# Kernel tuning notes

Hardware: AMD Instinct MI355X
Metric: run time of the kernel (lower is better)

The kernel has to match this reference:

```python
import jax, jax.numpy as jnp
import numpy as np

L = 4          # n_layers
HID = 64       # hidden_channels
MODES = 16     # n_modes
HEADS = 4      # n_heads
NP_SP = 500    # spatial engram patterns
NP_FR = 200    # spectral engram patterns
ED = 8         # embed_dim
WS = 4         # spatial window size
PRIME = 31.0


def setup_inputs() -> dict:
    key = jax.random.key(0)
    ks = jax.random.split(key, 20)
    B, Cin, Cout, S = 16, 3, 1, 16384
    f = lambda k, sh: jax.random.normal(k, sh, dtype=jnp.float32) * 0.05
    ch = HID // HEADS
    return {
        "x": jax.random.normal(ks[0], (B, Cin, S), dtype=jnp.float32),
        "lift_W": f(ks[1], (Cin, HID)), "lift_b": f(ks[2], (HID,)),
        "proj_W": f(ks[3], (HID, Cout)), "proj_b": f(ks[4], (Cout,)),
        "sp_emb": f(ks[5], (L, NP_SP, ED)), "sp_W": f(ks[6], (L, ED, HID)), "sp_b": f(ks[7], (L, HID)),
        "fr_emb": f(ks[8], (L, NP_FR, ED)), "fr_W": f(ks[9], (L, ED, HID * MODES)), "fr_b": f(ks[10], (L, HID * MODES)),
        "g_W1": f(ks[11], (L, 3 * HID, 64)), "g_b1": f(ks[12], (L, 64)),
        "g_W2": f(ks[13], (L, 64, 3)), "g_b2": f(ks[14], (L, 3)),
        "mhf_Wr": f(ks[15], (L, HEADS, ch, ch, MODES)),
        "mhf_Wi": f(ks[16], (L, HEADS, ch, ch, MODES)),
    }


def _spatial_engram(x, emb, W, b):
    # x: [B, C, S] -> hash each replicate-padded window of size WS -> embedding gather -> linear
    B, C, S = x.shape
    pad = WS // 2
    xp = jnp.pad(x, ((0, 0), (0, 0), (pad, pad)), mode='edge')   # [B, C, S+WS]
    sC = xp.sum(axis=1)                                          # [B, S+WS]
    # window sum over WS consecutive positions (vectorized over all seq positions)
    wsum = sC[:, 0:S] + sC[:, 1:S + 1] + sC[:, 2:S + 2] + sC[:, 3:S + 3]  # [B, S]
    idx = (wsum * PRIME).astype(jnp.int32) % NP_SP               # truncate-toward-zero like torch .long()
    idx = jnp.clip(idx, 0, NP_SP - 1)
    e = emb[idx]                                                 # [B, S, ED] gather
    out = e @ W + b                                              # [B, S, C]
    return out.transpose(0, 2, 1)                                # [B, C, S]


def _spectral_engram(x, emb, W, b):
    B, C, S = x.shape
    xf = jnp.fft.rfft(x, axis=-1)                                # [B, C, F]
    mag = jnp.abs(xf[:, :, :MODES]).mean(axis=1)                 # [B, MODES]
    idx = ((mag * 1000.0).astype(jnp.int32)).sum(axis=1) % NP_FR # [B]
    e = emb[idx]                                                 # [B, ED]
    proj = (e @ W + b).reshape(B, C, MODES)
    full = jnp.zeros((B, C, xf.shape[-1]), dtype=xf.dtype).at[:, :, :MODES].set(proj.astype(xf.dtype))
    return jnp.fft.irfft(full, n=S, axis=-1)


def _mhf_spectral_conv(x, Wr, Wi):
    # multi-head Fourier spectral conv: per-head complex channel mixing on low modes
    B, C, S = x.shape
    ch = C // HEADS
    xf = jnp.fft.rfft(x, axis=-1)                                # [B, C, F]
    xh = xf[:, :, :MODES].reshape(B, HEADS, ch, MODES)           # [B, H, ch, M]
    Wc = Wr + 1j * Wi                                            # [H, ch, ch, M]
    of = jnp.einsum('bhim,hiom->bhom', xh, Wc).reshape(B, C, MODES)
    full = jnp.zeros((B, C, xf.shape[-1]), dtype=xf.dtype).at[:, :, :MODES].set(of)
    return jnp.fft.irfft(full, n=S, axis=-1)


def _gated_fusion(sp, mh, fr, W1, b1, W2, b2):
    g = jnp.concatenate([sp.mean(-1), mh.mean(-1), fr.mean(-1)], axis=-1)  # [B, 3C]
    h = jax.nn.relu(g @ W1 + b1)
    w = jax.nn.softmax(h @ W2 + b2, axis=-1)                     # [B, 3]
    return (w[:, 0, None, None] * sp + w[:, 1, None, None] * mh + w[:, 2, None, None] * fr)


def reference(x, lift_W, lift_b, proj_W, proj_b, sp_emb, sp_W, sp_b,
              fr_emb, fr_W, fr_b, g_W1, g_b1, g_W2, g_b2, mhf_Wr, mhf_Wi):
    # lifting: [B, Cin, S] -> [B, HID, S]
    h = jnp.einsum('bcs,cd->bds', x, lift_W) + lift_b[None, :, None]
    for i in range(L):
        sp = _spatial_engram(h, sp_emb[i], sp_W[i], sp_b[i])
        mh = _mhf_spectral_conv(h, mhf_Wr[i], mhf_Wi[i])
        fr = _spectral_engram(h, fr_emb[i], fr_W[i], fr_b[i])
        h = _gated_fusion(sp, mh, fr, g_W1[i], g_b1[i], g_W2[i], g_b2[i])
        h = jax.nn.gelu(h, approximate=False)  # torch F.gelu default = exact erf
    out = jnp.einsum('bcs,cd->bds', h, proj_W) + proj_b[None, :, None]
    return out
```

## Files before the change

### kernel.cpp

```cpp
#include <hip/hip_runtime.h>
#include <math.h>

#define B_ 16
#define CIN_ 3
#define HID_ 64
#define S_ 16384
#define MODES_ 16
#define HEADS_ 4
#define CH_ 16
#define ED_ 8
#define NPSP_ 500
#define NPFR_ 200
#define LAYERS_ 4
#define RECW_ 34

__device__ __forceinline__ float gelu_f32(float v) {
    return 0.5f * v * (1.0f + erff(v * 0.70710678118654752f));
}

__device__ __constant__ double KC_[16] = {1.0, 0.99518472667219688624,
    0.98078528040323044913, 0.95694033573220886494, 0.92387953251128675613,
    0.88192126434835502971, 0.83146961230254523708, 0.77301045336273696081,
    0.70710678118654752440, 0.63439328416364549822, 0.55557023301960222474,
    0.47139673682599764856, 0.38268343236508977173, 0.29028467725446236764,
    0.19509032201612826785, 0.09801714032956060199};
__device__ __constant__ double KS_[16] = {0.0, 0.09801714032956060199,
    0.19509032201612826785, 0.29028467725446236764, 0.38268343236508977173,
    0.47139673682599764856, 0.55557023301960222474, 0.63439328416364549822,
    0.70710678118654752440, 0.77301045336273696081, 0.83146961230254523708,
    0.88192126434835502971, 0.92387953251128675613, 0.95694033573220886494,
    0.98078528040323044913, 0.99518472667219688624};

__global__ __launch_bounds__(256) void k_sptab(const float* __restrict__ sp_emb,
                                               const float* __restrict__ sp_W,
                                               float* __restrict__ T0f) {
    int lay = blockIdx.y;
    int tid = blockIdx.x * 256 + threadIdx.x;
    int c = tid & 63, id = tid >> 6;
    const float* e = sp_emb + (size_t)lay * NPSP_ * ED_ + (size_t)id * ED_;
    const float* w = sp_W + (size_t)lay * ED_ * HID_ + c;
    double a = 0.0;
#pragma unroll
    for (int k = 0; k < ED_; k++) a = fma((double)e[k], (double)w[k * HID_], a);
    T0f[((size_t)lay * HID_ + c) * NPSP_ + id] = (float)a;
}

__global__ __launch_bounds__(256) void k_lift(const float* __restrict__ x,
                                              const float* __restrict__ W,
                                              const float* __restrict__ bias,
                                              float* __restrict__ h,
                                              double* __restrict__ sC2) {
    int b = blockIdx.y;
    int s = blockIdx.x * 256 + threadIdx.x;
    const float* xb = x + (size_t)b * CIN_ * S_ + s;
    double x0 = (double)xb[0];
    double x1 = (double)xb[S_];
    double x2 = (double)xb[2 * S_];
    float* hb = h + (size_t)b * HID_ * S_ + s;
#pragma unroll
    for (int q = 0; q < 4; ++q) {
        double a = 0.0;
        for (int dd = 0; dd < 16; ++dd) {
            int d = q * 16 + dd;
            double v = x0 * (double)W[d];
            v = fma(x1, (double)W[HID_ + d], v);
            v = fma(x2, (double)W[2 * HID_ + d], v);
            v += (double)bias[d];
            hb[(size_t)d * S_] = (float)v;
            a += v;
        }
        sC2[(size_t)(q * B_ + b) * S_ + s] = a;
    }
}

__global__ __launch_bounds__(256) void k_hash(const double* __restrict__ sC2,
                                              const float* __restrict__ emb_l,
                                              int* __restrict__ idx,
                                              double* __restrict__ Eb) {
    int b = blockIdx.y;
    int s0 = blockIdx.x * 256;
    int t = threadIdx.x;
    __shared__ double sl[260];
    for (int j = t; j < 260; j += 256) {
        int p = s0 - 2 + j;
        p = p < 0 ? 0 : (p > S_ - 1 ? S_ - 1 : p);
        const double* sb = sC2 + (size_t)b * S_ + p;
        sl[j] = ((sb[0] + sb[(size_t)B_ * S_]) + sb[(size_t)2 * B_ * S_])
                + sb[(size_t)3 * B_ * S_];
    }
    __syncthreads();
    double wsum = ((sl[t] + sl[t + 1]) + sl[t + 2]) + sl[t + 3];
    int ti = (int)(wsum * 31.0);
    int id = ti % NPSP_;
    if (id < 0) id += NPSP_;
    idx[(size_t)b * S_ + s0 + t] = id;

    const float* er = emb_l + id * ED_;
    double ev[8];
#pragma unroll
    for (int k = 0; k < 8; k++) ev[k] = (double)er[k];

    int lane = t & 63, wv = t >> 6;
    __shared__ double red[4][8];
#pragma unroll
    for (int k = 0; k < 8; k++) {
        double v = ev[k];
        for (int off = 32; off > 0; off >>= 1) v += __shfl_down(v, off, 64);
        if (lane == 0) red[wv][k] = v;
    }
    __syncthreads();
    if (t < 8) {
        double v = red[0][t] + red[1][t] + red[2][t] + red[3][t];
        atomicAdd(&Eb[b * ED_ + t], v);
    }
}

__global__ __launch_bounds__(256, 4) void k_dft(const float* __restrict__ h,
                                                double* __restrict__ Xr,
                                                double* __restrict__ Xi) {
    int b = blockIdx.y;
    int c0 = blockIdx.x >> 1;
    int mlo = (blockIdx.x & 1) * 8;
    int t = threadIdx.x;
    const float* h0 = h + ((size_t)(b * HID_ + c0)) * S_ + t;

    double acc[16];
#pragma unroll
    for (int k = 0; k < 16; k++) acc[k] = 0.0;

    double c1 = cospi((double)t / 8192.0);
    double s1 = sinpi((double)t / 8192.0);
    double cmv[8], smv[8];
    {
        double cc_ = 1.0, ss_ = 0.0;
        for (int j = 0; j < mlo; j++) {
            double nc = cc_ * c1 - ss_ * s1;
            double ns = ss_ * c1 + cc_ * s1;
            cc_ = nc; ss_ = ns;
        }
#pragma unroll
        for (int mi = 0; mi < 8; mi++) {
            cmv[mi] = cc_; smv[mi] = ss_;
            double nc = cc_ * c1 - ss_ * s1;
            double ns = ss_ * c1 + cc_ * s1;
            cc_ = nc; ss_ = ns;
        }
    }

    for (int k = 0; k < 16; k++) {
        int s = k << 8;
        double a0 = (double)h0[s];
        double b0 = (double)h0[s + 4096];
        double c0v = (double)h0[s + 8192];
        double d0 = (double)h0[s + 12288];

        double t10 = a0 + c0v, t20 = b0 + d0;
        double g00 = t10 + t20, g20 = t10 - t20;
        double ar0 = a0 - c0v, br0 = b0 - d0;

        if (mlo == 0) {
            acc[0] += g00;
        }
#pragma unroll
        for (int mi = 0; mi < 8; mi++) {
            if (mlo == 0 && mi == 0) continue;
            double c = cmv[mi], s_ = smv[mi];
            if ((mi & 1) == 0) {
                double g0x = (mi & 2) ? g20 : g00;
                acc[mi]     = fma(g0x, c,  acc[mi]);
                acc[8 + mi] = fma(g0x, s_, acc[8 + mi]);
            } else if ((mi & 2) == 0) {
                acc[mi]     = fma(ar0, c,  fma(-br0, s_, acc[mi]));
                acc[8 + mi] = fma(ar0, s_, fma( br0, c,  acc[8 + mi]));
            } else {
                acc[mi]     = fma(ar0, c,  fma( br0, s_, acc[mi]));
                acc[8 + mi] = fma(ar0, s_, fma(-br0, c,  acc[8 + mi]));
            }
        }
#pragma unroll
        for (int mi = 0; mi < 8; mi++) {
            int m = mlo + mi;
            double cn = cmv[mi] * KC_[m] - smv[mi] * KS_[m];
            double sn = smv[mi] * KC_[m] + cmv[mi] * KS_[m];
            cmv[mi] = cn; smv[mi] = sn;
        }
    }

    int lane = t & 63, wv = t >> 6;
    __shared__ double red[4][16];
#pragma unroll
    for (int k = 0; k < 16; k++) {
        double v = acc[k];
        for (int off = 32; off > 0; off >>= 1) v += __shfl_down(v, off, 64);
        if (lane == 0) red[wv][k] = v;
    }
    __syncthreads();
    if (t < 16) {
        double v = ((red[0][t] + red[1][t]) + red[2][t]) + red[3][t];
        int im = t >> 3, mi = t & 7;
        size_t o = ((size_t)b * HID_ + c0) * MODES_ + mlo + mi;
        if (im) Xi[o] = -v;
        else    Xr[o] = v;
    }
}

__global__ __launch_bounds__(256) void k_gate(const double* __restrict__ Xr,
                                              const double* __restrict__ Xi,
                                              const float* __restrict__ mWr,
                                              const float* __restrict__ mWi,
                                              const float* __restrict__ fr_emb_l,
                                              const float* __restrict__ fr_W_l,
                                              const float* __restrict__ fr_b_l,
                                              const double* __restrict__ Eb,
                                              const float* __restrict__ sp_W_l,
                                              const float* __restrict__ sp_b_l,
                                              const float* __restrict__ gW1,
                                              const float* __restrict__ gb1,
                                              const float* __restrict__ gW2,
                                              const float* __restrict__ gb2,
                                              float* __restrict__ RECg) {
    int b = blockIdx.x;
    int t = threadIdx.x;
    __shared__ double sXr[1024], sXi[1024];
    __shared__ double sMr[1024], sMi[1024], sP[1024];
    __shared__ double gg[192], h1s[64], sww[3];
    __shared__ int magI[MODES_];
    __shared__ int fidxS;

    for (int j = t; j < 1024; j += 256) {
        sXr[j] = Xr[(size_t)b * 1024 + j];
        sXi[j] = Xi[(size_t)b * 1024 + j];
    }
    __syncthreads();

    if (t < MODES_) {
        double acc = 0.0;
        for (int c = 0; c < HID_; c++) {
            double re = sXr[c * MODES_ + t];
            double im = sXi[c * MODES_ + t];
            acc += sqrt(re * re + im * im);
        }
        magI[t] = (int)(acc * (1.0 / 64.0) * 1000.0);
    }

    for (int u = t; u < 1024; u += 256) {
        int hh = u >> 8, rem = u & 255, o = rem >> 4, m = rem & 15;
        const float* wr = mWr + (size_t)hh * CH_ * CH_ * MODES_;
        const float* wi = mWi + (size_t)hh * CH_ * CH_ * MODES_;
        double aR = 0.0, aI = 0.0;
#pragma unroll 4
        for (int i = 0; i < CH_; i++) {
            double xrv = sXr[(hh * CH_ + i) * MODES_ + m];
            double xiv = sXi[(hh * CH_ + i) * MODES_ + m];
            double wrv = (double)wr[(i * CH_ + o) * MODES_ + m];
            double wiv = (double)wi[(i * CH_ + o) * MODES_ + m];
            aR += xrv * wrv - xiv * wiv;
            aI += xrv * wiv + xiv * wrv;
        }
        sMr[(hh * CH_ + o) * MODES_ + m] = aR;
        sMi[(hh * CH_ + o) * MODES_ + m] = aI;
    }
    __syncthreads();

    if (t == 0) {
        int ssum = 0;
        for (int m = 0; m < MODES_; m++) ssum += magI[m];
        int f = ssum % NPFR_;
        if (f < 0) f += NPFR_;
        fidxS = f;
    }
    __syncthreads();

    {
        const float* fe = fr_emb_l + fidxS * ED_;
        for (int u = t; u < 1024; u += 256) {
            double acc = 0.0;
            for (int e = 0; e < ED_; e++)
                acc += (double)fe[e] * (double)fr_W_l[e * 1024 + u];
            sP[u] = acc + (double)fr_b_l[u];
        }
    }
    __syncthreads();

    if (t < 64) {
        double a = 0.0;
        for (int e = 0; e < ED_; e++)
            a += Eb[b * ED_ + e] * (double)sp_W_l[e * 64 + t];
        gg[t]       = a * (1.0 / 16384.0) + (double)sp_b_l[t];
        gg[64 + t]  = sMr[t * MODES_] * (1.0 / 16384.0);
        gg[128 + t] = sP[t * MODES_] * (1.0 / 16384.0);
    }
    __syncthreads();
    if (t < 64) {
        double a = 0.0;
        for (int k = 0; k < 192; k++) a += gg[k] * (double)gW1[k * 64 + t];
        a += (double)gb1[t];
        h1s[t] = a > 0.0 ? a : 0.0;
    }
    __syncthreads();
    if (t == 0) {
        double l[3];
        for (int j = 0; j < 3; j++) {
            double a = 0.0;
            for (int k = 0; k < 64; k++) a += h1s[k] * (double)gW2[k * 3 + j];
            l[j] = a + (double)gb2[j];
        }
        double mx = fmax(l[0], fmax(l[1], l[2]));
        double e0 = exp(l[0] - mx), e1 = exp(l[1] - mx), e2 = exp(l[2] - mx);
        double sum = e0 + e1 + e2;
        sww[0] = e0 / sum; sww[1] = e1 / sum; sww[2] = e2 / sum;
    }
    __syncthreads();

    double w0s = sww[0], w1s = sww[1], w2s = sww[2];
    float* R = RECg + (size_t)b * HID_ * RECW_;
    for (int u = t; u < 1024; u += 256) {
        int c = u >> 4, m = u & 15;
        double km = (m == 0 ? 1.0 : 2.0) * (1.0 / 16384.0);
        R[c * RECW_ + 2 * m]     = (float)(km * (w1s * sMr[u] + w2s * sP[u]));
        R[c * RECW_ + 2 * m + 1] = (m == 0) ? 0.0f : (float)(-(km * w1s * sMi[u]));
    }
    if (t < 64) {
        R[t * RECW_ + 32] = (float)(w0s * (double)sp_b_l[t]);
        R[t * RECW_ + 33] = (float)w0s;
    }
}

__global__ __launch_bounds__(256, 4) void k_recon(const int* __restrict__ idx,
                                                  const float* __restrict__ T0f_l,
                                                  const float* __restrict__ RECg,
                                                  float* __restrict__ h,
                                                  double* __restrict__ sC2) {
    int b = blockIdx.y;
    int cz = blockIdx.z;
    int cbase = cz * 16;
    int s0 = blockIdx.x * 256 + threadIdx.x;
    int t = threadIdx.x;
    __shared__ __align__(16) float sT[16 * NPSP_];
    {
        const float4* src = reinterpret_cast<const float4*>(T0f_l + (size_t)cbase * NPSP_);
        float4* dst = reinterpret_cast<float4*>(sT);
        for (int j = t; j < 16 * NPSP_ / 4; j += 256) dst[j] = src[j];
    }
    __syncthreads();

    int id0 = idx[(size_t)b * S_ + s0];
    int id1 = idx[(size_t)b * S_ + s0 + 4096];
    int id2 = idx[(size_t)b * S_ + s0 + 8192];
    int id3 = idx[(size_t)b * S_ + s0 + 12288];

    double cb = cospi((double)s0 / 8192.0);
    double sb = sinpi((double)s0 / 8192.0);
    double cmd = 1.0, smd = 0.0;
    float cm[16], sm[16];
    cm[0] = 1.0f; sm[0] = 0.0f;
#pragma unroll
    for (int m = 1; m < 16; m++) {
        double nc = cmd * cb - smd * sb;
        double ns = smd * cb + cmd * sb;
        cmd = nc; smd = ns;
        cm[m] = (float)cmd; sm[m] = (float)smd;
    }

    const float* Rb = RECg + ((size_t)b * HID_ + cbase) * RECW_;
    float w0g = Rb[33];
    float* hb = h + (size_t)b * HID_ * S_ + (size_t)cbase * S_;
    double cs0 = 0.0, cs1 = 0.0, cs2 = 0.0, cs3 = 0.0;
#pragma unroll 2
    for (int c = 0; c < 16; c++) {
        const float2* r2 = (const float2*)(Rb + (size_t)c * RECW_);
        const float* tc = sT + c * NPSP_;
        float bias = Rb[(size_t)c * RECW_ + 32];
        float p0 = fmaf(w0g, tc[id0], bias);
        float p1 = fmaf(w0g, tc[id1], bias);
        float p2 = fmaf(w0g, tc[id2], bias);
        float p3 = fmaf(w0g, tc[id3], bias);
        float PA = 0.0f, PB = 0.0f, PC = 0.0f, PD = 0.0f, QB = 0.0f, QD = 0.0f;
#pragma unroll
        for (int mm = 0; mm < 16; mm += 4) {
            float2 q0 = r2[mm], q1 = r2[mm + 1], q2 = r2[mm + 2], q3 = r2[mm + 3];
            PA = fmaf(q0.x, cm[mm], PA);     PA = fmaf(q0.y, sm[mm], PA);
            PB = fmaf(q1.x, cm[mm + 1], PB); PB = fmaf(q1.y, sm[mm + 1], PB);
            QB = fmaf(q1.y, cm[mm + 1], QB); QB = fmaf(-q1.x, sm[mm + 1], QB);
            PC = fmaf(q2.x, cm[mm + 2], PC); PC = fmaf(q2.y, sm[mm + 2], PC);
            PD = fmaf(q3.x, cm[mm + 3], PD); PD = fmaf(q3.y, sm[mm + 3], PD);
            QD = fmaf(q3.y, cm[mm + 3], QD); QD = fmaf(-q3.x, sm[mm + 3], QD);
        }
        float u0 = PA + PC, u1 = PA - PC;
        float w0 = PB + PD, qd = QB - QD;
        float g0 = gelu_f32(p0 + (u0 + w0));
        float g1 = gelu_f32(p1 + (u1 + qd));
        float g2 = gelu_f32(p2 + (u0 - w0));
        float g3 = gelu_f32(p3 + (u1 - qd));
        hb[(size_t)c * S_ + s0]         = g0;
        hb[(size_t)c * S_ + s0 + 4096]  = g1;
        hb[(size_t)c * S_ + s0 + 8192]  = g2;
        hb[(size_t)c * S_ + s0 + 12288] = g3;
        cs0 += (double)g0; cs1 += (double)g1;
        cs2 += (double)g2; cs3 += (double)g3;
    }
    double* sc = sC2 + (size_t)(cz * B_ + b) * S_;
    sc[s0]         = cs0;
    sc[s0 + 4096]  = cs1;
    sc[s0 + 8192]  = cs2;
    sc[s0 + 12288] = cs3;
}

__global__ __launch_bounds__(256) void k_proj(const float* __restrict__ h,
                                              const float* __restrict__ pW,
                                              const float* __restrict__ pb,
                                              float* __restrict__ out) {
    int b = blockIdx.y;
    int s = blockIdx.x * 256 + threadIdx.x;
    const float* hb = h + (size_t)b * HID_ * S_ + s;
    double acc = 0.0;
    for (int d = 0; d < HID_; d++)
        acc += (double)hb[(size_t)d * S_] * (double)pW[d];
    out[(size_t)b * S_ + s] = (float)(acc + (double)pb[0]);
}

extern "C" void kernel_launch(void* const* d_in, const int* in_sizes, int n_in,
                              void* d_out, int out_size, void* d_ws, size_t ws_size,
                              hipStream_t stream) {
    const float* x      = (const float*)d_in[0];
    const float* lift_W = (const float*)d_in[1];
    const float* lift_b = (const float*)d_in[2];
    const float* proj_W = (const float*)d_in[3];
    const float* proj_b = (const float*)d_in[4];
    const float* sp_emb = (const float*)d_in[5];
    const float* sp_W   = (const float*)d_in[6];
    const float* sp_b   = (const float*)d_in[7];
    const float* fr_emb = (const float*)d_in[8];
    const float* fr_W   = (const float*)d_in[9];
    const float* fr_b   = (const float*)d_in[10];
    const float* g_W1   = (const float*)d_in[11];
    const float* g_b1   = (const float*)d_in[12];
    const float* g_W2   = (const float*)d_in[13];
    const float* g_b2   = (const float*)d_in[14];
    const float* mhf_Wr = (const float*)d_in[15];
    const float* mhf_Wi = (const float*)d_in[16];

    char* ws = (char*)d_ws;
    float* h    = (float*)ws;   ws += (size_t)B_ * HID_ * S_ * 4;
    double* sC2 = (double*)ws;  ws += (size_t)4 * B_ * S_ * 8;
    int* idx    = (int*)ws;     ws += (size_t)B_ * S_ * 4;
    double* Xr  = (double*)ws;  ws += (size_t)B_ * HID_ * MODES_ * 8;
    double* Xi  = (double*)ws;  ws += (size_t)B_ * HID_ * MODES_ * 8;
    float* REC  = (float*)ws;   ws += (size_t)B_ * HID_ * RECW_ * 4;
    double* Eb  = (double*)ws;  ws += (size_t)LAYERS_ * B_ * ED_ * 8;
    float* T0f  = (float*)ws;   ws += (size_t)LAYERS_ * HID_ * NPSP_ * 4;

    hipMemsetAsync(Eb, 0, (size_t)LAYERS_ * B_ * ED_ * 8, stream);

    dim3 blk(256);
    k_sptab<<<dim3(NPSP_ * HID_ / 256, LAYERS_), blk, 0, stream>>>(sp_emb, sp_W, T0f);
    k_lift<<<dim3(S_ / 256, B_), blk, 0, stream>>>(x, lift_W, lift_b, h, sC2);

    for (int lay = 0; lay < LAYERS_; ++lay) {
        k_hash<<<dim3(S_ / 256, B_), blk, 0, stream>>>(
            sC2, sp_emb + (size_t)lay * NPSP_ * ED_, idx, Eb + (size_t)lay * B_ * ED_);
        k_dft<<<dim3(HID_ * 2, B_), blk, 0, stream>>>(h, Xr, Xi);
        k_gate<<<dim3(B_), blk, 0, stream>>>(
            Xr, Xi,
            mhf_Wr + (size_t)lay * HEADS_ * CH_ * CH_ * MODES_,
            mhf_Wi + (size_t)lay * HEADS_ * CH_ * CH_ * MODES_,
            fr_emb + (size_t)lay * NPFR_ * ED_,
            fr_W + (size_t)lay * ED_ * HID_ * MODES_,
            fr_b + (size_t)lay * HID_ * MODES_,
            Eb + (size_t)lay * B_ * ED_,
            sp_W + (size_t)lay * ED_ * HID_,
            sp_b + (size_t)lay * HID_,
            g_W1 + (size_t)lay * 192 * 64,
            g_b1 + (size_t)lay * 64,
            g_W2 + (size_t)lay * 64 * 3,
            g_b2 + (size_t)lay * 3,
            REC);
        k_recon<<<dim3(S_ / 1024, B_, 4), blk, 0, stream>>>(
            idx, T0f + (size_t)lay * HID_ * NPSP_, REC, h, sC2);
    }

    k_proj<<<dim3(S_ / 256, B_), blk, 0, stream>>>(h, proj_W, proj_b, (float*)d_out);
}
```

Measured before the change: 494.4 us.

## Factor DFT twiddles into per-block constants and one per-thread post-rotation

The truncated DFT kernel now computes all 16 modes in one block instead of splitting them across two blocks, which halves the number of blocks and the global reads of h. Inside the loop, the twiddles are reduced to compile-time constants indexed by k*m. This works because each thread's stride of 256 samples makes the phase a multiple of 2*pi/64. A single complex rotation by the thread's own phase is applied after the loop, replacing the per-iteration recurrence updates. The cost is 32 double accumulators per thread, which raises register pressure and may lower occupancy, and the larger shuffle reduction adds some work.

New measurement: 877.9 us. 1.78x slower.

```diff
diff --git a/kernel.cpp b/kernel.cpp
--- a/kernel.cpp
+++ b/kernel.cpp
@@ -30,6 +30,19 @@
     0.70710678118654752440, 0.77301045336273696081, 0.83146961230254523708,
     0.88192126434835502971, 0.92387953251128675613, 0.95694033573220886494,
     0.98078528040323044913, 0.99518472667219688624};
+
+__device__ __forceinline__ double cos32(int j) {
+    j &= 63;
+    int r = j & 15, q = j >> 4;
+    double kc = KC_[r], ks = KS_[r];
+    return q == 0 ? kc : (q == 1 ? -ks : (q == 2 ? -kc : ks));
+}
+__device__ __forceinline__ double sin32(int j) {
+    j &= 63;
+    int r = j & 15, q = j >> 4;
+    double kc = KC_[r], ks = KS_[r];
+    return q == 0 ? ks : (q == 1 ? kc : (q == 2 ? -ks : -kc));
+}
 
 __global__ __launch_bounds__(256) void k_sptab(const float* __restrict__ sp_emb,
                                                const float* __restrict__ sp_W,
@@ -119,34 +132,15 @@
                                                 double* __restrict__ Xr,
                                                 double* __restrict__ Xi) {
     int b = blockIdx.y;
-    int c0 = blockIdx.x >> 1;
-    int mlo = (blockIdx.x & 1) * 8;
+    int c0 = blockIdx.x;
     int t = threadIdx.x;
     const float* h0 = h + ((size_t)(b * HID_ + c0)) * S_ + t;
 
-    double acc[16];
-#pragma unroll
-    for (int k = 0; k < 16; k++) acc[k] = 0.0;
-
-    double c1 = cospi((double)t / 8192.0);
-    double s1 = sinpi((double)t / 8192.0);
-    double cmv[8], smv[8];
-    {
-        double cc_ = 1.0, ss_ = 0.0;
-        for (int j = 0; j < mlo; j++) {
-            double nc = cc_ * c1 - ss_ * s1;
-            double ns = ss_ * c1 + cc_ * s1;
-            cc_ = nc; ss_ = ns;
-        }
-#pragma unroll
-        for (int mi = 0; mi < 8; mi++) {
-            cmv[mi] = cc_; smv[mi] = ss_;
-            double nc = cc_ * c1 - ss_ * s1;
-            double ns = ss_ * c1 + cc_ * s1;
-            cc_ = nc; ss_ = ns;
-        }
-    }
-
+    double acc[32];
+#pragma unroll
+    for (int k = 0; k < 32; k++) acc[k] = 0.0;
+
+#pragma unroll
     for (int k = 0; k < 16; k++) {
         int s = k << 8;
         double a0 = (double)h0[s];
@@ -158,47 +152,52 @@
         double g00 = t10 + t20, g20 = t10 - t20;
         double ar0 = a0 - c0v, br0 = b0 - d0;
 
-        if (mlo == 0) {
-            acc[0] += g00;
-        }
-#pragma unroll
-        for (int mi = 0; mi < 8; mi++) {
-            if (mlo == 0 && mi == 0) continue;
-            double c = cmv[mi], s_ = smv[mi];
-            if ((mi & 1) == 0) {
-                double g0x = (mi & 2) ? g20 : g00;
-                acc[mi]     = fma(g0x, c,  acc[mi]);
-                acc[8 + mi] = fma(g0x, s_, acc[8 + mi]);
-            } else if ((mi & 2) == 0) {
-                acc[mi]     = fma(ar0, c,  fma(-br0, s_, acc[mi]));
-                acc[8 + mi] = fma(ar0, s_, fma( br0, c,  acc[8 + mi]));
+#pragma unroll
+        for (int m = 0; m < 16; m++) {
+            const double cphi = cos32(k * m);
+            const double sphi = sin32(k * m);
+            if ((m & 1) == 0) {
+                double gv = (m & 2) ? g20 : g00;
+                acc[m]      = fma(gv, cphi, acc[m]);
+                acc[16 + m] = fma(gv, sphi, acc[16 + m]);
+            } else if ((m & 2) == 0) {
+                acc[m]      = fma(ar0, cphi, fma(-br0, sphi, acc[m]));
+                acc[16 + m] = fma(ar0, sphi, fma( br0, cphi, acc[16 + m]));
             } else {
-                acc[mi]     = fma(ar0, c,  fma( br0, s_, acc[mi]));
-                acc[8 + mi] = fma(ar0, s_, fma(-br0, c,  acc[8 + mi]));
+                acc[m]      = fma(ar0, cphi, fma( br0, sphi, acc[m]));
+                acc[16 + m] = fma(ar0, sphi, fma(-br0, cphi, acc[16 + m]));
             }
         }
-#pragma unroll
-        for (int mi = 0; mi < 8; mi++) {
-            int m = mlo + mi;
-            double cn = cmv[mi] * KC_[m] - smv[mi] * KS_[m];
-            double sn = smv[mi] * KC_[m] + cmv[mi] * KS_[m];
-            cmv[mi] = cn; smv[mi] = sn;
+    }
+
+    {
+        double c1 = cospi((double)t / 8192.0);
+        double s1 = sinpi((double)t / 8192.0);
+        double ct = 1.0, st = 0.0;
+#pragma unroll
+        for (int m = 0; m < 16; m++) {
+            double ure = acc[m], uim = acc[16 + m];
+            acc[m]      = ure * ct - uim * st;
+            acc[16 + m] = ure * st + uim * ct;
+            double nc = ct * c1 - st * s1;
+            double ns = st * c1 + ct * s1;
+            ct = nc; st = ns;
         }
     }
 
     int lane = t & 63, wv = t >> 6;
-    __shared__ double red[4][16];
-#pragma unroll
-    for (int k = 0; k < 16; k++) {
+    __shared__ double red[4][32];
+#pragma unroll
+    for (int k = 0; k < 32; k++) {
         double v = acc[k];
         for (int off = 32; off > 0; off >>= 1) v += __shfl_down(v, off, 64);
         if (lane == 0) red[wv][k] = v;
     }
     __syncthreads();
-    if (t < 16) {
+    if (t < 32) {
         double v = ((red[0][t] + red[1][t]) + red[2][t]) + red[3][t];
-        int im = t >> 3, mi = t & 7;
-        size_t o = ((size_t)b * HID_ + c0) * MODES_ + mlo + mi;
+        int im = t >> 4, m = t & 15;
+        size_t o = ((size_t)b * HID_ + c0) * MODES_ + m;
         if (im) Xi[o] = -v;
         else    Xr[o] = v;
     }
@@ -459,7 +458,7 @@
     for (int lay = 0; lay < LAYERS_; ++lay) {
         k_hash<<<dim3(S_ / 256, B_), blk, 0, stream>>>(
             sC2, sp_emb + (size_t)lay * NPSP_ * ED_, idx, Eb + (size_t)lay * B_ * ED_);
-        k_dft<<<dim3(HID_ * 2, B_), blk, 0, stream>>>(h, Xr, Xi);
+        k_dft<<<dim3(HID_, B_), blk, 0, stream>>>(h, Xr, Xi);
         k_gate<<<dim3(B_), blk, 0, stream>>>(
             Xr, Xi,
             mhf_Wr + (size_t)lay * HEADS_ * CH_ * CH_ * MODES_,
```
